# Kernel tuning notes

Hardware: AMD Instinct MI355X
Metric: run time of the kernel (lower is better)

## Reference

```python
import jax, jax.numpy as jnp
import numpy as np

B, L, DIN = 16, 1024, 512
H, DH = 4, 128          # num_heads = 4, head_dim = in_features // 4
DEG = 16                # avg random in-degree (plus one self-loop per node)
NEG_SLOPE = 0.2         # DGL GATConv default leaky_relu slope


def setup_inputs() -> dict:
    key = jax.random.key(0)
    ks = jax.random.split(key, 8)
    N = B * L
    E = N * DEG
    src = jax.random.randint(ks[0], (E,), 0, N)
    dst = jax.random.randint(ks[1], (E,), 0, N)
    loops = jnp.arange(N)
    src = jnp.concatenate([src, loops])  # self-loops guarantee every dst has in-edges
    dst = jnp.concatenate([dst, loops])
    s = 1.0 / np.sqrt(DIN)
    text = jax.random.normal(ks[2], (B, L, DIN), jnp.float32)
    weight = jax.random.normal(ks[3], (DIN, DIN), jnp.float32) * s      # module's self.weight
    fc_w = jax.random.normal(ks[4], (DIN, H * DH), jnp.float32) * s     # GATConv fc (no bias)
    attn_l = jax.random.normal(ks[5], (H, DH), jnp.float32) * s
    attn_r = jax.random.normal(ks[6], (H, DH), jnp.float32) * s
    bias = jax.random.normal(ks[7], (DIN,), jnp.float32) * 0.01         # module's self.bias
    return {"text": text, "weight": weight, "fc_w": fc_w,
            "attn_l": attn_l, "attn_r": attn_r, "bias": bias,
            "src": src, "dst": dst}


def reference(text, weight, fc_w, attn_l, attn_r, bias, src, dst):
    b, l, d = text.shape
    N = b * l
    # outer linear projection
    hidden = jnp.einsum('bld,de->ble', text, weight)
    feat = hidden.reshape(N, d)
    # GATConv: fc projection to heads
    h = (feat @ fc_w).reshape(N, H, DH)                 # [N, H, DH]
    el = jnp.einsum('nhd,hd->nh', h, attn_l)            # [N, H]
    er = jnp.einsum('nhd,hd->nh', h, attn_r)            # [N, H]
    # edge attention logits (src contributes el, dst contributes er)
    e = jax.nn.leaky_relu(el[src] + er[dst], NEG_SLOPE)  # [E, H]
    # segment (per-destination) softmax, numerically stable
    emax = jax.ops.segment_max(e, dst, num_segments=N)   # [N, H]
    ex = jnp.exp(e - emax[dst])
    denom = jax.ops.segment_sum(ex, dst, num_segments=N)
    alpha = ex / denom[dst]                              # [E, H]
    # weighted message aggregation (scatter-add)
    m = h[src] * alpha[:, :, None]                       # [E, H, DH]
    out = jax.ops.segment_sum(m, dst, num_segments=N)    # [N, H, DH]
    return out.reshape(b, l, H * DH) + bias
```

## Files before the change

kernel.cpp:

```cpp
#include <hip/hip_runtime.h>
#include <stdint.h>

#define AS1 __attribute__((address_space(1)))
#define AS3 __attribute__((address_space(3)))

typedef __attribute__((ext_vector_type(8))) short short8;
typedef __attribute__((ext_vector_type(4))) float f32x4;

#define CAP 64
#define NGEMM 512
#define NSCAT 128
#define NW2T 256
#define NCVT 2048

__device__ __forceinline__ short f2bf(float f) {
  union { float f; unsigned u; } v; v.f = f;
  unsigned r = v.u + 0x7fffu + ((v.u >> 16) & 1u);
  return (short)(r >> 16);
}
__device__ __forceinline__ float bf_lo(unsigned w) { union { unsigned u; float f; } v; v.u = w << 16;          return v.f; }
__device__ __forceinline__ float bf_hi(unsigned w) { union { unsigned u; float f; } v; v.u = w & 0xffff0000u;  return v.f; }

__global__ __launch_bounds__(256) void k_w2t_cvt(const float* __restrict__ W,
                                                 const float* __restrict__ F,
                                                 const float* __restrict__ text,
                                                 short* __restrict__ W2t,
                                                 short* __restrict__ textb,
                                                 int* __restrict__ cnt) {
  const int tid = threadIdx.x;
  const int b   = blockIdx.x;

  if (b >= NW2T) {
    const size_t base = (size_t)(b - NW2T) * 4096 + tid * 16;
    const float4* p = (const float4*)(text + base);
    float4 a0 = p[0], a1 = p[1], a2 = p[2], a3 = p[3];
    short8 o0, o1;
    o0[0] = f2bf(a0.x); o0[1] = f2bf(a0.y); o0[2] = f2bf(a0.z); o0[3] = f2bf(a0.w);
    o0[4] = f2bf(a1.x); o0[5] = f2bf(a1.y); o0[6] = f2bf(a1.z); o0[7] = f2bf(a1.w);
    o1[0] = f2bf(a2.x); o1[1] = f2bf(a2.y); o1[2] = f2bf(a2.z); o1[3] = f2bf(a2.w);
    o1[4] = f2bf(a3.x); o1[5] = f2bf(a3.y); o1[6] = f2bf(a3.z); o1[7] = f2bf(a3.w);
    *(short8*)(textb + base) = o0;
    *(short8*)(textb + base + 8) = o1;
    return;
  }

  if (tid < 64) cnt[b * 64 + tid] = 0;

  __shared__ float sW[64][36];
  __shared__ float sF[64][36];
  const int bx = b & 15, by = b >> 4;
  const int d0 = bx * 32, j0 = by * 32;
  const int dx = tid & 15, jy = tid >> 4;
  float a00 = 0.f, a01 = 0.f, a10 = 0.f, a11 = 0.f;
  const int wr = tid >> 3, wc = (tid & 7) * 8;
  const int fr = tid >> 2, fc = (tid & 3) * 8;
  for (int e0 = 0; e0 < 512; e0 += 64) {
    float4 w0 = *(const float4*)&W[(size_t)(d0 + wr) * 512 + e0 + wc];
    float4 w1 = *(const float4*)&W[(size_t)(d0 + wr) * 512 + e0 + wc + 4];
    float4 f0 = *(const float4*)&F[(size_t)(e0 + fr) * 512 + j0 + fc];
    float4 f1 = *(const float4*)&F[(size_t)(e0 + fr) * 512 + j0 + fc + 4];
    sW[wc + 0][wr] = w0.x; sW[wc + 1][wr] = w0.y; sW[wc + 2][wr] = w0.z; sW[wc + 3][wr] = w0.w;
    sW[wc + 4][wr] = w1.x; sW[wc + 5][wr] = w1.y; sW[wc + 6][wr] = w1.z; sW[wc + 7][wr] = w1.w;
    *(float4*)&sF[fr][fc] = f0;
    *(float4*)&sF[fr][fc + 4] = f1;
    __syncthreads();
#pragma unroll
    for (int e = 0; e < 64; ++e) {
      float2 w2 = *(const float2*)&sW[e][dx * 2];
      float2 f2 = *(const float2*)&sF[e][jy * 2];
      a00 += w2.x * f2.x; a01 += w2.x * f2.y;
      a10 += w2.y * f2.x; a11 += w2.y * f2.y;
    }
    __syncthreads();
  }
  short* o0 = W2t + (size_t)(j0 + jy * 2) * 512 + d0 + dx * 2;
  o0[0] = f2bf(a00); o0[1] = f2bf(a10);
  o0[512] = f2bf(a01); o0[513] = f2bf(a11);
}

__global__ __launch_bounds__(256) void k_gemm_scatter(const short* __restrict__ A,
                                                      const short* __restrict__ Bt,
                                                      short* __restrict__ Cs,
                                                      float* __restrict__ el,
                                                      float* __restrict__ er,
                                                      const float* __restrict__ attn_l,
                                                      const float* __restrict__ attn_r,
                                                      const int* __restrict__ src,
                                                      const int* __restrict__ dst,
                                                      int* __restrict__ cnt,
                                                      int* __restrict__ bucket,
                                                      int E, int N) {
  const int tid = threadIdx.x;
  if (blockIdx.x >= NGEMM) {
    for (int e = (blockIdx.x - NGEMM) * 256 + tid; e < E; e += NSCAT * 256) {
      int d = dst[e];
      int p = atomicAdd(&cnt[d], 1);
      if (p < CAP) bucket[(size_t)d * CAP + p] = src[e];
    }
    return;
  }

  __shared__ __align__(16) short sA[2][128 * 64];
  __shared__ __align__(16) short sB[2][128 * 64];
  __shared__ float sEl[128][2];
  __shared__ float sEr[128][2];
  const int bx   = blockIdx.x;
  const int xcd  = bx & 7, kk = bx >> 3;
  const int bm0  = (xcd * 16 + (kk & 15)) * 128;
  const int hh   = kk >> 4;
  const int bn0  = hh * 128;
  const int lane = tid & 63;
  const int wid  = tid >> 6;
  const int wm   = wid >> 1;
  const int wn   = wid & 1;
  const int cc   = lane & 15;

  f32x4 acc[4][4] = {};

  const int srow  = tid >> 3;
  const int sslot = (tid & 7) ^ (srow & 7);
  const int lslot = tid & 7;

#pragma unroll
  for (int r = 0; r < 4; ++r) {
    int row = r * 32 + srow;
    __builtin_amdgcn_global_load_lds((const AS1 void*)(A + (size_t)(bm0 + row) * 512 + sslot * 8),
                                     (AS3 void*)(sA[0] + row * 64 + lslot * 8), 16, 0, 0);
    __builtin_amdgcn_global_load_lds((const AS1 void*)(Bt + (size_t)(bn0 + row) * 512 + sslot * 8),
                                     (AS3 void*)(sB[0] + row * 64 + lslot * 8), 16, 0, 0);
  }
  __syncthreads();

  for (int kt = 0; kt < 8; ++kt) {
    const int cur = kt & 1;
    if (kt < 7) {
      const int kbase = (kt + 1) * 64;
#pragma unroll
      for (int r = 0; r < 4; ++r) {
        int row = r * 32 + srow;
        __builtin_amdgcn_global_load_lds((const AS1 void*)(A + (size_t)(bm0 + row) * 512 + kbase + sslot * 8),
                                         (AS3 void*)(sA[cur ^ 1] + row * 64 + lslot * 8), 16, 0, 0);
        __builtin_amdgcn_global_load_lds((const AS1 void*)(Bt + (size_t)(bn0 + row) * 512 + kbase + sslot * 8),
                                         (AS3 void*)(sB[cur ^ 1] + row * 64 + lslot * 8), 16, 0, 0);
      }
    }
#pragma unroll
    for (int ks = 0; ks < 2; ++ks) {
      short8 af[4], bfr[4];
#pragma unroll
      for (int i = 0; i < 4; ++i) {
        int row  = wm * 64 + i * 16 + cc;
        int slot = (ks * 4 + (lane >> 4)) ^ (row & 7);
        af[i] = *(const short8*)(sA[cur] + row * 64 + slot * 8);
      }
#pragma unroll
      for (int j = 0; j < 4; ++j) {
        int row  = wn * 64 + j * 16 + cc;
        int slot = (ks * 4 + (lane >> 4)) ^ (row & 7);
        bfr[j] = *(const short8*)(sB[cur] + row * 64 + slot * 8);
      }
#pragma unroll
      for (int i = 0; i < 4; ++i)
#pragma unroll
        for (int j = 0; j < 4; ++j)
          acc[i][j] = __builtin_amdgcn_mfma_f32_16x16x32_bf16(af[i], bfr[j], acc[i][j], 0, 0, 0);
    }
    __syncthreads();
  }

  const int r4 = (lane >> 4) * 4;
#pragma unroll
  for (int i = 0; i < 4; ++i)
#pragma unroll
    for (int j = 0; j < 4; ++j) {
      int cin = wn * 64 + j * 16 + cc;
#pragma unroll
      for (int rg = 0; rg < 4; ++rg) {
        int gr = bm0 + wm * 64 + i * 16 + r4 + rg;
        Cs[((size_t)hh * N + gr) * 128 + cin] = f2bf(acc[i][j][rg]);
      }
    }
  float alv[4], arv[4];
#pragma unroll
  for (int j = 0; j < 4; ++j) {
    int cl = wn * 64 + j * 16 + cc;
    alv[j] = attn_l[hh * 128 + cl];
    arv[j] = attn_r[hh * 128 + cl];
  }
#pragma unroll
  for (int i = 0; i < 4; ++i)
#pragma unroll
    for (int rg = 0; rg < 4; ++rg) {
      float pl = 0.f, pr = 0.f;
#pragma unroll
      for (int j = 0; j < 4; ++j) {
        float v = acc[i][j][rg];
        pl += v * alv[j]; pr += v * arv[j];
      }
#pragma unroll
      for (int d = 1; d < 16; d <<= 1) {
        pl += __shfl_xor(pl, d);
        pr += __shfl_xor(pr, d);
      }
      if (cc == 0) {
        int row = wm * 64 + i * 16 + r4 + rg;
        sEl[row][wn] = pl;
        sEr[row][wn] = pr;
      }
    }
  __syncthreads();
  if (tid < 128) {
    int gr = bm0 + tid;
    el[gr * 4 + hh] = sEl[tid][0] + sEl[tid][1];
    er[gr * 4 + hh] = sEr[tid][0] + sEr[tid][1];
  }
}

__global__ __launch_bounds__(256) void k_aggregate(const int* __restrict__ cnt, const int* __restrict__ bucket,
                                                   const float* __restrict__ el, const float* __restrict__ er,
                                                   const short* __restrict__ hs, const float* __restrict__ bias,
                                                   float* __restrict__ out, int N) {
  const int b    = blockIdx.x;
  const int s    = (b >> 1) & 3;
  const int nt   = (b >> 3) * 2 + (b & 1);
  const int nd   = nt * 4 + (threadIdx.x >> 6);
  const int lane = threadIdx.x & 63;
  const int g    = lane >> 4;
  const int cl   = lane & 15;

  int n = cnt[nd]; n = (n < CAP) ? n : CAP;
  const int* bk = bucket + (size_t)nd * CAP;

  int l   = (lane < n) ? lane : (n - 1);
  int idx = bk[l];
  float ern = er[nd * 4 + s];
  float x = el[idx * 4 + s] + ern;
  x = (x > 0.f) ? x : 0.2f * x;
  float wgt = (lane < n) ? __expf(x) : 0.f;
  float ssum = wgt;
#pragma unroll
  for (int d = 1; d < 64; d <<= 1) ssum += __shfl_xor(ssum, d);

  const short* hbase = hs + (size_t)s * N * 128;
  float acc[8];
#pragma unroll
  for (int j = 0; j < 8; ++j) acc[j] = 0.f;

  for (int base = 0; base < n; base += 8) {
    int e0 = base + g, e1 = base + 4 + g;
    int s0 = __shfl(idx, e0), s1 = __shfl(idx, e1);
    float w0 = __shfl(wgt, e0), w1 = __shfl(wgt, e1);
    uint4 v0 = ((const uint4*)(hbase + (size_t)s0 * 128))[cl];
    uint4 v1 = ((const uint4*)(hbase + (size_t)s1 * 128))[cl];
    acc[0] += w0 * bf_lo(v0.x) + w1 * bf_lo(v1.x);
    acc[1] += w0 * bf_hi(v0.x) + w1 * bf_hi(v1.x);
    acc[2] += w0 * bf_lo(v0.y) + w1 * bf_lo(v1.y);
    acc[3] += w0 * bf_hi(v0.y) + w1 * bf_hi(v1.y);
    acc[4] += w0 * bf_lo(v0.z) + w1 * bf_lo(v1.z);
    acc[5] += w0 * bf_hi(v0.z) + w1 * bf_hi(v1.z);
    acc[6] += w0 * bf_lo(v0.w) + w1 * bf_lo(v1.w);
    acc[7] += w0 * bf_hi(v0.w) + w1 * bf_hi(v1.w);
  }

#pragma unroll
  for (int d = 16; d < 64; d <<= 1) {
#pragma unroll
    for (int j = 0; j < 8; ++j) acc[j] += __shfl_xor(acc[j], d);
  }

  if (g == 0) {
    float inv = 1.f / ssum;
    int c0 = s * 128 + cl * 8;
    float4 b0 = *(const float4*)(bias + c0);
    float4 b1 = *(const float4*)(bias + c0 + 4);
    float4 o0, o1;
    o0.x = acc[0] * inv + b0.x; o0.y = acc[1] * inv + b0.y;
    o0.z = acc[2] * inv + b0.z; o0.w = acc[3] * inv + b0.w;
    o1.x = acc[4] * inv + b1.x; o1.y = acc[5] * inv + b1.y;
    o1.z = acc[6] * inv + b1.z; o1.w = acc[7] * inv + b1.w;
    float* op = out + (size_t)nd * 512 + c0;
    *(float4*)op = o0;
    *(float4*)(op + 4) = o1;
  }
}

extern "C" void kernel_launch(void* const* d_in, const int* in_sizes, int n_in,
                              void* d_out, int out_size, void* d_ws, size_t ws_size,
                              hipStream_t stream) {
  const float* text   = (const float*)d_in[0];
  const float* weight = (const float*)d_in[1];
  const float* fcw    = (const float*)d_in[2];
  const float* attn_l = (const float*)d_in[3];
  const float* attn_r = (const float*)d_in[4];
  const float* bias   = (const float*)d_in[5];
  const int*   src    = (const int*)d_in[6];
  const int*   dst    = (const int*)d_in[7];
  const int E = in_sizes[6];
  const int N = in_sizes[0] / 512;

  char* ws = (char*)d_ws;
  size_t o = 0;
  auto carve = [&](size_t bytes) { void* p = ws + o; o = (o + bytes + 255) & ~(size_t)255; return p; };
  short* w2t    = (short*)carve((size_t)512 * 512 * 2);
  short* textb  = (short*)carve((size_t)N * 512 * 2);
  short* hs     = (short*)carve((size_t)N * 512 * 2);
  float* el     = (float*)carve((size_t)N * 4 * 4);
  float* er     = (float*)carve((size_t)N * 4 * 4);
  int*   cnt    = (int*)carve((size_t)N * 4);
  int*   bucket = (int*)carve((size_t)N * CAP * 4);

  k_w2t_cvt<<<NW2T + NCVT, 256, 0, stream>>>(weight, fcw, text, w2t, textb, cnt);
  k_gemm_scatter<<<NGEMM + NSCAT, 256, 0, stream>>>(textb, w2t, hs, el, er, attn_l, attn_r,
                                                    src, dst, cnt, bucket, E, N);
  k_aggregate<<<N * 4 / 4, 256, 0, stream>>>(cnt, bucket, el, er, hs, bias, (float*)d_out, N);
}
```

Before: 84.96 us.

## Fuse fp32-to-bf16 text conversion into GEMM A-tile loading

Removes the separate text-to-bf16 conversion pass and its intermediate buffer. The GEMM now loads fp32 text into registers, converts it, and writes the swizzled bf16 into LDS after the MFMA work for the current tile, while B keeps using direct global-to-LDS loads. This saves one full write and read of the bf16 text copy. In exchange, each GEMM block reads twice the A bytes (fp32) once per head tile, so text is read four times as fp32, and register pressure goes up from holding the prefetched floats.

New measurement: 97.38 us. +14.6%, slower.

```diff
diff --git a/kernel.cpp b/kernel.cpp
--- a/kernel.cpp
+++ b/kernel.cpp
@@ -10,8 +10,6 @@
 #define CAP 64
 #define NGEMM 512
 #define NSCAT 128
-#define NW2T 256
-#define NCVT 2048
 
 __device__ __forceinline__ short f2bf(float f) {
   union { float f; unsigned u; } v; v.f = f;
@@ -21,29 +19,12 @@
 __device__ __forceinline__ float bf_lo(unsigned w) { union { unsigned u; float f; } v; v.u = w << 16;          return v.f; }
 __device__ __forceinline__ float bf_hi(unsigned w) { union { unsigned u; float f; } v; v.u = w & 0xffff0000u;  return v.f; }
 
-__global__ __launch_bounds__(256) void k_w2t_cvt(const float* __restrict__ W,
-                                                 const float* __restrict__ F,
-                                                 const float* __restrict__ text,
-                                                 short* __restrict__ W2t,
-                                                 short* __restrict__ textb,
-                                                 int* __restrict__ cnt) {
+__global__ __launch_bounds__(256) void k_w2t(const float* __restrict__ W,
+                                             const float* __restrict__ F,
+                                             short* __restrict__ W2t,
+                                             int* __restrict__ cnt) {
   const int tid = threadIdx.x;
   const int b   = blockIdx.x;
-
-  if (b >= NW2T) {
-    const size_t base = (size_t)(b - NW2T) * 4096 + tid * 16;
-    const float4* p = (const float4*)(text + base);
-    float4 a0 = p[0], a1 = p[1], a2 = p[2], a3 = p[3];
-    short8 o0, o1;
-    o0[0] = f2bf(a0.x); o0[1] = f2bf(a0.y); o0[2] = f2bf(a0.z); o0[3] = f2bf(a0.w);
-    o0[4] = f2bf(a1.x); o0[5] = f2bf(a1.y); o0[6] = f2bf(a1.z); o0[7] = f2bf(a1.w);
-    o1[0] = f2bf(a2.x); o1[1] = f2bf(a2.y); o1[2] = f2bf(a2.z); o1[3] = f2bf(a2.w);
-    o1[4] = f2bf(a3.x); o1[5] = f2bf(a3.y); o1[6] = f2bf(a3.z); o1[7] = f2bf(a3.w);
-    *(short8*)(textb + base) = o0;
-    *(short8*)(textb + base + 8) = o1;
-    return;
-  }
-
   if (tid < 64) cnt[b * 64 + tid] = 0;
 
   __shared__ float sW[64][36];
@@ -78,7 +59,7 @@
   o0[512] = f2bf(a01); o0[513] = f2bf(a11);
 }
 
-__global__ __launch_bounds__(256) void k_gemm_scatter(const short* __restrict__ A,
+__global__ __launch_bounds__(256) void k_gemm_scatter(const float* __restrict__ A32,
                                                       const short* __restrict__ Bt,
                                                       short* __restrict__ Cs,
                                                       float* __restrict__ el,
@@ -120,29 +101,53 @@
   const int srow  = tid >> 3;
   const int sslot = (tid & 7) ^ (srow & 7);
   const int lslot = tid & 7;
-
-#pragma unroll
-  for (int r = 0; r < 4; ++r) {
-    int row = r * 32 + srow;
-    __builtin_amdgcn_global_load_lds((const AS1 void*)(A + (size_t)(bm0 + row) * 512 + sslot * 8),
-                                     (AS3 void*)(sA[0] + row * 64 + lslot * 8), 16, 0, 0);
-    __builtin_amdgcn_global_load_lds((const AS1 void*)(Bt + (size_t)(bn0 + row) * 512 + sslot * 8),
-                                     (AS3 void*)(sB[0] + row * 64 + lslot * 8), 16, 0, 0);
-  }
+  const int arow  = tid >> 1;
+  const int ahalf = tid & 1;
+
+  float4 f[8];
+
+#define LOAD_A(KT)                                                                   \
+  {                                                                                  \
+    const float4* gA = (const float4*)(A32 + (size_t)(bm0 + arow) * 512 + (KT) * 64 + ahalf * 32); \
+    _Pragma("unroll")                                                                \
+    for (int s = 0; s < 8; ++s) f[s] = gA[s];                                        \
+  }
+
+#define WRITE_A(BUF)                                                                 \
+  {                                                                                  \
+    _Pragma("unroll")                                                                \
+    for (int s = 0; s < 4; ++s) {                                                    \
+      short8 v;                                                                      \
+      v[0] = f2bf(f[2 * s].x); v[1] = f2bf(f[2 * s].y);                              \
+      v[2] = f2bf(f[2 * s].z); v[3] = f2bf(f[2 * s].w);                              \
+      v[4] = f2bf(f[2 * s + 1].x); v[5] = f2bf(f[2 * s + 1].y);                      \
+      v[6] = f2bf(f[2 * s + 1].z); v[7] = f2bf(f[2 * s + 1].w);                      \
+      int slot = (ahalf * 4 + s) ^ (arow & 7);                                       \
+      *(short8*)((BUF) + arow * 64 + slot * 8) = v;                                  \
+    }                                                                                \
+  }
+
+#define STAGE_B(KT, BUF)                                                             \
+  {                                                                                  \
+    _Pragma("unroll")                                                                \
+    for (int r = 0; r < 4; ++r) {                                                    \
+      int row = r * 32 + srow;                                                       \
+      __builtin_amdgcn_global_load_lds(                                              \
+          (const AS1 void*)(Bt + (size_t)(bn0 + row) * 512 + (KT) * 64 + sslot * 8), \
+          (AS3 void*)((BUF) + row * 64 + lslot * 8), 16, 0, 0);                      \
+    }                                                                                \
+  }
+
+  LOAD_A(0)
+  STAGE_B(0, sB[0])
+  WRITE_A(sA[0])
   __syncthreads();
 
   for (int kt = 0; kt < 8; ++kt) {
     const int cur = kt & 1;
     if (kt < 7) {
-      const int kbase = (kt + 1) * 64;
-#pragma unroll
-      for (int r = 0; r < 4; ++r) {
-        int row = r * 32 + srow;
-        __builtin_amdgcn_global_load_lds((const AS1 void*)(A + (size_t)(bm0 + row) * 512 + kbase + sslot * 8),
-                                         (AS3 void*)(sA[cur ^ 1] + row * 64 + lslot * 8), 16, 0, 0);
-        __builtin_amdgcn_global_load_lds((const AS1 void*)(Bt + (size_t)(bn0 + row) * 512 + kbase + sslot * 8),
-                                         (AS3 void*)(sB[cur ^ 1] + row * 64 + lslot * 8), 16, 0, 0);
-      }
+      LOAD_A(kt + 1)
+      STAGE_B(kt + 1, sB[cur ^ 1])
     }
 #pragma unroll
     for (int ks = 0; ks < 2; ++ks) {
@@ -164,6 +169,9 @@
 #pragma unroll
         for (int j = 0; j < 4; ++j)
           acc[i][j] = __builtin_amdgcn_mfma_f32_16x16x32_bf16(af[i], bfr[j], acc[i][j], 0, 0, 0);
+    }
+    if (kt < 7) {
+      WRITE_A(sA[cur ^ 1])
     }
     __syncthreads();
   }
@@ -302,15 +310,14 @@
   size_t o = 0;
   auto carve = [&](size_t bytes) { void* p = ws + o; o = (o + bytes + 255) & ~(size_t)255; return p; };
   short* w2t    = (short*)carve((size_t)512 * 512 * 2);
-  short* textb  = (short*)carve((size_t)N * 512 * 2);
   short* hs     = (short*)carve((size_t)N * 512 * 2);
   float* el     = (float*)carve((size_t)N * 4 * 4);
   float* er     = (float*)carve((size_t)N * 4 * 4);
   int*   cnt    = (int*)carve((size_t)N * 4);
   int*   bucket = (int*)carve((size_t)N * CAP * 4);
 
-  k_w2t_cvt<<<NW2T + NCVT, 256, 0, stream>>>(weight, fcw, text, w2t, textb, cnt);
-  k_gemm_scatter<<<NGEMM + NSCAT, 256, 0, stream>>>(textb, w2t, hs, el, er, attn_l, attn_r,
+  k_w2t<<<256, 256, 0, stream>>>(weight, fcw, w2t, cnt);
+  k_gemm_scatter<<<NGEMM + NSCAT, 256, 0, stream>>>(text, w2t, hs, el, er, attn_l, attn_r,
                                                     src, dst, cnt, bucket, E, N);
   k_aggregate<<<N * 4 / 4, 256, 0, stream>>>(cnt, bucket, el, er, hs, bias, (float*)d_out, N);
 }
```
